# Kernel optimization log

Hardware: AMD Instinct MI355X
Metric: run time of the kernel (lower is better)

Reference implementation:

```python
import jax, jax.numpy as jnp
import numpy as np

ALPHA = 0.2  # LeakyReLU negative slope


def setup_inputs() -> dict:
    key = jax.random.key(0)
    k1, k2, k3, k4 = jax.random.split(key, 4)
    B, N, F_IN, F_OUT = 4, 4096, 256, 256
    h = jax.random.normal(k1, (B, N, F_IN), dtype=jnp.float32)
    adj = jax.random.randint(k2, (B, N, N), 0, 2, dtype=jnp.int32)
    # xavier_normal with gain=1.414: std = gain*sqrt(2/(fan_in+fan_out))
    std_W = 1.414 * np.sqrt(2.0 / (F_IN + F_OUT))
    W = jax.random.normal(k3, (F_IN, F_OUT), dtype=jnp.float32) * std_W
    std_a = 1.414 * np.sqrt(2.0 / (1 + 2 * F_OUT))
    a = jax.random.normal(k4, (1, 2 * F_OUT), dtype=jnp.float32) * std_a
    return {"h": h, "adj": adj, "W": W, "a": a}


def reference(h, adj, W, a):
    # h: [B, N, F_in], adj: [B, N, N] (0/1), W: [F_in, F_out], a: [1, 2*F_out]
    F_out = W.shape[1]
    Hh = jnp.einsum('bni,io->bno', h, W)               # [B, N, F_out]
    a_src = a[0, :F_out]                                # attends to edge source i
    a_dst = a[0, F_out:]                                # attends to edge target j
    s = jnp.einsum('bno,o->bn', Hh, a_src)              # [B, N]
    d = jnp.einsum('bno,o->bn', Hh, a_dst)              # [B, N]
    # score(i,j) = a . concat(Hh_i, Hh_j) = s_i + d_j
    logits = s[:, :, None] + d[:, None, :]              # [B, N, N]
    # edge_e = exp(-leakyrelu(score)) only on edges (adj nonzero), else 0
    e = jnp.where(adj != 0,
                  jnp.exp(-jax.nn.leaky_relu(logits, negative_slope=ALPHA)),
                  jnp.zeros((), dtype=Hh.dtype))        # [B, N, N]
    rowsum = jnp.sum(e, axis=-1, keepdims=True)         # [B, N, 1]
    # rows with zero sum keep divisor 1 (as in the torch code)
    rowsum = jnp.where(rowsum == 0.0, 1.0, rowsum)
    h_prime = jnp.einsum('bnm,bmo->bno', e, Hh) / rowsum  # [B, N, F_out]
    return jax.nn.elu(h_prime)  # concat=True branch
```

## Files before the change

kernel.cpp:

```cpp
#include <hip/hip_runtime.h>

#define LRELU_ALPHA 0.2f

typedef __bf16 bf16x8 __attribute__((ext_vector_type(8)));
typedef unsigned short u16;
typedef unsigned short u16x4v __attribute__((ext_vector_type(4)));
typedef unsigned short u16x8 __attribute__((ext_vector_type(8)));
typedef float f32x4 __attribute__((ext_vector_type(4)));
typedef int int4v __attribute__((ext_vector_type(4)));
typedef unsigned int u32;
typedef unsigned long long u64;

__device__ __forceinline__ u16 f2bf(float f) {
  unsigned int u = __float_as_uint(f);
  u += 0x7fffu + ((u >> 16) & 1u);
  return (u16)(u >> 16);
}

__device__ __forceinline__ void gload16(const void* g, void* lds) {
  __builtin_amdgcn_global_load_lds(
      (const __attribute__((address_space(1))) void*)g,
      (__attribute__((address_space(3))) void*)lds, 16, 0, 0);
}

__global__ __launch_bounds__(256) void wcast(const float* __restrict__ W,
                                             u16* __restrict__ WbT) {
  int idx = blockIdx.x * 256 + threadIdx.x;
  WbT[idx] = f2bf(W[(idx & 255) * 256 + (idx >> 8)]);
}

__global__ __launch_bounds__(256) void packadj(const int* __restrict__ adj,
                                               u32* __restrict__ maskg) {
  const int tid = threadIdx.x;
  const int l = tid & 63, w = tid >> 6;
  const size_t row = (size_t)blockIdx.x * 4 + w;
  const int* arow = adj + row * 4096;
  u64* mrow = (u64*)(maskg + row * 128);
  for (int it = 0; it < 16; ++it) {
    const int* base = arow + it * 256;
    int v0 = base[l], v1 = base[l + 64], v2 = base[l + 128], v3 = base[l + 192];
    u64 b0 = __ballot(v0 != 0);
    u64 b1 = __ballot(v1 != 0);
    u64 b2 = __ballot(v2 != 0);
    u64 b3 = __ballot(v3 != 0);
    if (l == 0) {
      mrow[it * 4 + 0] = b0;
      mrow[it * 4 + 1] = b1;
      mrow[it * 4 + 2] = b2;
      mrow[it * 4 + 3] = b3;
    }
  }
}

__global__ __launch_bounds__(256) void gemm1(const float* __restrict__ h,
                                             const u16* __restrict__ WbT,
                                             const float* __restrict__ a,
                                             u16* __restrict__ HhTt,
                                             float* __restrict__ sbuf,
                                             float* __restrict__ dbuf) {
  const int tid = threadIdx.x, bid = blockIdx.x;
  const int l = tid & 63, w = tid >> 6;
  const int lr = l & 15;
  const int lk = (l >> 4) << 3;
  const int rowA = bid * 64 + 16 * w + lr;
  const float* hrow = h + (size_t)rowA * 256 + lk;

  f32x4 acc[16];
#pragma unroll
  for (int n = 0; n < 16; ++n) acc[n] = (f32x4){0.f, 0.f, 0.f, 0.f};

  for (int k0 = 0; k0 < 256; k0 += 32) {
    f32x4 a0 = *(const f32x4*)(hrow + k0);
    f32x4 a1 = *(const f32x4*)(hrow + k0 + 4);
    u16x8 au;
    au[0] = f2bf(a0[0]); au[1] = f2bf(a0[1]); au[2] = f2bf(a0[2]); au[3] = f2bf(a0[3]);
    au[4] = f2bf(a1[0]); au[5] = f2bf(a1[1]); au[6] = f2bf(a1[2]); au[7] = f2bf(a1[3]);
    bf16x8 af = __builtin_bit_cast(bf16x8, au);
#pragma unroll
    for (int n = 0; n < 16; ++n) {
      int4v bv = *(const int4v*)(WbT + (size_t)(16 * n + lr) * 256 + k0 + lk);
      bf16x8 bf = __builtin_bit_cast(bf16x8, bv);
      acc[n] = __builtin_amdgcn_mfma_f32_16x16x32_bf16(af, bf, acc[n], 0, 0, 0);
    }
  }

  float sp[4] = {0.f, 0.f, 0.f, 0.f}, dp[4] = {0.f, 0.f, 0.f, 0.f};
#pragma unroll
  for (int n = 0; n < 16; ++n) {
    int col = 16 * n + lr;
    float as = a[col];
    float ad = a[256 + col];
#pragma unroll
    for (int rr = 0; rr < 4; ++rr) {
      int row = bid * 64 + 16 * w + ((l >> 4) << 2) + rr;
      int bb = row >> 12, kk = row & 4095;
      float v = acc[n][rr];
      size_t addr = (size_t)bb * 1048576 + (size_t)(kk >> 5) * 8192 +
                    (col >> 4) * 512 + ((kk >> 3) & 3) * 128 + (col & 15) * 8 +
                    (kk & 7);
      HhTt[addr] = f2bf(v);
      sp[rr] += v * as;
      dp[rr] += v * ad;
    }
  }
#pragma unroll
  for (int rr = 0; rr < 4; ++rr) {
#pragma unroll
    for (int off = 1; off < 16; off <<= 1) {
      sp[rr] += __shfl_xor(sp[rr], off);
      dp[rr] += __shfl_xor(dp[rr], off);
    }
  }
  if ((l & 15) == 0) {
#pragma unroll
    for (int rr = 0; rr < 4; ++rr) {
      int row = bid * 64 + 16 * w + ((l >> 4) << 2) + rr;
      sbuf[row] = sp[rr];
      dbuf[row] = dp[rr];
    }
  }
}

__global__ __launch_bounds__(256, 2) void gat_main(const u32* __restrict__ maskg,
                                                   const u16* __restrict__ HhTt,
                                                   const float* __restrict__ s,
                                                   const float* __restrict__ d,
                                                   float* __restrict__ out) {
  __shared__ __align__(16) u16 Bt[3][8192];
  __shared__ __align__(16) u16 At[2][1024];
  __shared__ __align__(16) u32 Mk[4096];
  __shared__ __align__(16) float Dt[3][32];
  __shared__ float rs_lds[32];

  const int tid = threadIdx.x, bid = blockIdx.x;
  const int xcd = bid & 7;
  const int t512 = (xcd << 6) | (bid >> 3);
  const int b = t512 >> 7;
  const int rowbase = (t512 & 127) << 5;

  const int l = tid & 63, w = tid >> 6;
  const int lr = l & 15, lkg = l >> 4;
  const int er = tid >> 3, c8 = tid & 7;

  {
    const u32* mrow = maskg + ((size_t)(b * 4096 + rowbase)) * 128;
    const int r = tid >> 3;
    const int w0 = (tid & 7) * 16;
#pragma unroll
    for (int j = 0; j < 16; ++j) {
      int ww = w0 + j;
      Mk[r * 128 + ((ww + r) & 127)] = mrow[r * 128 + ww];
    }
  }

  const float s_e = s[b * 4096 + rowbase + er];

  const char* bsrcB = (const char*)HhTt + (size_t)b * 2097152 + l * 16;
  const char* dsrcB = (const char*)d + (size_t)b * 16384 + w * 32 + l * 16;
  char* BtB = (char*)&Bt[0][0];
  char* DtB = (char*)&Dt[0][0];

  const int atoff0 = lr * 32 + lkg * 8;
  const int atoff1 = (16 + lr) * 32 + lkg * 8;
  const int btbase = (w * 4) * 512 + lkg * 128 + lr * 8;

  f32x4 acc0[4], acc1[4];
#pragma unroll
  for (int n = 0; n < 4; ++n) {
    acc0[n] = (f32x4){0.f, 0.f, 0.f, 0.f};
    acc1[n] = (f32x4){0.f, 0.f, 0.f, 0.f};
  }
  float racc = 0.f;

#define ISSUE_B(BUF, STEP)                                                    \
  {                                                                           \
    const size_t so_ = (size_t)(STEP) * 16384;                                \
    gload16(bsrcB + so_ + (w * 4 + 0) * 1024,                                 \
            BtB + (BUF) * 16384 + (w * 4 + 0) * 1024);                        \
    gload16(bsrcB + so_ + (w * 4 + 1) * 1024,                                 \
            BtB + (BUF) * 16384 + (w * 4 + 1) * 1024);                        \
    gload16(bsrcB + so_ + (w * 4 + 2) * 1024,                                 \
            BtB + (BUF) * 16384 + (w * 4 + 2) * 1024);                        \
    gload16(bsrcB + so_ + (w * 4 + 3) * 1024,                                 \
            BtB + (BUF) * 16384 + (w * 4 + 3) * 1024);                        \
  }

#define ISSUE_D(STEP)                                                         \
  {                                                                           \
    const int dst_ = (STEP) > 127 ? 127 : (STEP);                             \
    if (l < 2) gload16(dsrcB + (size_t)dst_ * 128,                            \
                       DtB + (dst_ % 3) * 128 + w * 32 + l * 16);             \
  }

#define EGEN(BA, STEP)                                                        \
  {                                                                           \
    u32 mword = Mk[er * 128 + (((STEP) + er) & 127)];                         \
    u32 m4 = mword >> (c8 * 4);                                               \
    f32x4 dv = *(const f32x4*)(DtB + ((STEP) % 3) * 128 + c8 * 16);           \
    u16x4v ev;                                                                \
    _Pragma("unroll")                                                         \
    for (int j = 0; j < 4; ++j) {                                             \
      float lg = s_e + dv[j];                                                 \
      float t = fmaxf(lg, LRELU_ALPHA * lg);                                  \
      float e = ((m4 >> j) & 1) ? __expf(-t) : 0.f;                           \
      racc += e;                                                              \
      ev[j] = f2bf(e);                                                        \
    }                                                                         \
    *(u16x4v*)&At[BA][er * 32 + c8 * 4] = ev;                                 \
  }

#define COMPUTE(BB, BA)                                                       \
  {                                                                           \
    bf16x8 af0 = __builtin_bit_cast(bf16x8, *(const int4v*)&At[BA][atoff0]);  \
    bf16x8 af1 = __builtin_bit_cast(bf16x8, *(const int4v*)&At[BA][atoff1]);  \
    __builtin_amdgcn_s_setprio(1);                                            \
    _Pragma("unroll")                                                         \
    for (int n = 0; n < 4; ++n) {                                             \
      bf16x8 bfv = __builtin_bit_cast(bf16x8,                                 \
          *(const int4v*)&Bt[BB][btbase + n * 512]);                          \
      acc0[n] = __builtin_amdgcn_mfma_f32_16x16x32_bf16(af0, bfv, acc0[n],    \
                                                        0, 0, 0);             \
      acc1[n] = __builtin_amdgcn_mfma_f32_16x16x32_bf16(af1, bfv, acc1[n],    \
                                                        0, 0, 0);             \
    }                                                                         \
    __builtin_amdgcn_s_setprio(0);                                            \
  }

#define SUBSTEP(J, BB, BA, BI, BAN)                                           \
  {                                                                           \
    ISSUE_B(BI, (J) + 2)                                                      \
    ISSUE_D((J) + 3)                                                          \
    EGEN(BAN, (J) + 1)                                                        \
    COMPUTE(BB, BA)                                                           \
    asm volatile("s_waitcnt lgkmcnt(0)" ::: "memory");                        \
    asm volatile("s_waitcnt vmcnt(5)" ::: "memory");                          \
    __builtin_amdgcn_s_barrier();                                             \
  }

  ISSUE_B(0, 0)
  ISSUE_B(1, 1)
  ISSUE_D(1)
  ISSUE_D(2)
  f32x4 d0v = *(const f32x4*)(d + b * 4096 + c8 * 4);
  __syncthreads();
  {
    u32 mword = Mk[er * 128 + (er & 127)];
    u32 m4 = mword >> (c8 * 4);
    u16x4v ev;
#pragma unroll
    for (int j = 0; j < 4; ++j) {
      float lg = s_e + d0v[j];
      float t = fmaxf(lg, LRELU_ALPHA * lg);
      float e = ((m4 >> j) & 1) ? __expf(-t) : 0.f;
      racc += e;
      ev[j] = f2bf(e);
    }
    *(u16x4v*)&At[0][er * 32 + c8 * 4] = ev;
  }
  asm volatile("s_waitcnt lgkmcnt(0)" ::: "memory");
  __builtin_amdgcn_s_barrier();

  for (int k = 0; k < 126; k += 6) {
    SUBSTEP(k + 0, 0, 0, 2, 1)
    SUBSTEP(k + 1, 1, 1, 0, 0)
    SUBSTEP(k + 2, 2, 0, 1, 1)
    SUBSTEP(k + 3, 0, 1, 2, 0)
    SUBSTEP(k + 4, 1, 0, 0, 1)
    SUBSTEP(k + 5, 2, 1, 1, 0)
  }
  EGEN(1, 127)
  COMPUTE(0, 0)
  asm volatile("s_waitcnt lgkmcnt(0)" ::: "memory");
  asm volatile("s_waitcnt vmcnt(0)" ::: "memory");
  __builtin_amdgcn_s_barrier();
  COMPUTE(1, 1)
#undef ISSUE_B
#undef ISSUE_D
#undef EGEN
#undef COMPUTE
#undef SUBSTEP

  racc += __shfl_xor(racc, 1);
  racc += __shfl_xor(racc, 2);
  racc += __shfl_xor(racc, 4);
  if (c8 == 0) rs_lds[er] = (racc == 0.f) ? 1.f : racc;
  __syncthreads();

#pragma unroll
  for (int t16 = 0; t16 < 2; ++t16) {
#pragma unroll
    for (int n = 0; n < 4; ++n) {
#pragma unroll
      for (int reg = 0; reg < 4; ++reg) {
        int rloc = 16 * t16 + lkg * 4 + reg;
        int col = w * 64 + 16 * n + lr;
        float v = (t16 ? acc1[n][reg] : acc0[n][reg]) / rs_lds[rloc];
        out[((size_t)(b * 4096 + rowbase + rloc)) * 256 + col] =
            v > 0.f ? v : (__expf(v) - 1.f);
      }
    }
  }
}

extern "C" void kernel_launch(void* const* d_in, const int* in_sizes, int n_in,
                              void* d_out, int out_size, void* d_ws, size_t ws_size,
                              hipStream_t stream) {
  const float* h = (const float*)d_in[0];
  const int* adj = (const int*)d_in[1];
  const float* W = (const float*)d_in[2];
  const float* a = (const float*)d_in[3];
  float* out = (float*)d_out;

  u16* WbT   = (u16*)d_ws;
  u16* HhTt  = (u16*)((char*)d_ws + 131072);
  float* sb  = (float*)((char*)d_ws + 131072 + 8388608);
  float* db  = sb + 16384;
  u32* maskg = (u32*)((char*)d_ws + 131072 + 8388608 + 131072);

  hipLaunchKernelGGL(wcast,    dim3(256),  dim3(256), 0, stream, W, WbT);
  hipLaunchKernelGGL(packadj,  dim3(4096), dim3(256), 0, stream, adj, maskg);
  hipLaunchKernelGGL(gemm1,    dim3(256),  dim3(256), 0, stream, h, WbT, a, HhTt, sb, db);
  hipLaunchKernelGGL(gat_main, dim3(512),  dim3(256), 0, stream, maskg, HhTt, sb, db, out);
}
```

Baseline: 170.2 us.

## Retile attention kernel to 64-row by 128-column panels and merge W cast into adjacency packing

The main attention kernel now tiles each block as 64 rows by 128 output columns instead of 32 rows by 256 columns. Each block computes twice as many attention weights per column-half, and each thread builds 8 weights per step. The change halves the B-tile staging per step and enlarges the mask and A buffers, trading duplicated exp work across the two column halves for less feature-tile traffic and a different LDS footprint. The W transpose/cast kernel is also folded into the adjacency-packing launch as extra blocks, removing one kernel launch.

```diff
diff --git a/kernel.cpp b/kernel.cpp
--- a/kernel.cpp
+++ b/kernel.cpp
@@ -4,7 +4,6 @@
 
 typedef __bf16 bf16x8 __attribute__((ext_vector_type(8)));
 typedef unsigned short u16;
-typedef unsigned short u16x4v __attribute__((ext_vector_type(4)));
 typedef unsigned short u16x8 __attribute__((ext_vector_type(8)));
 typedef float f32x4 __attribute__((ext_vector_type(4)));
 typedef int int4v __attribute__((ext_vector_type(4)));
@@ -23,15 +22,16 @@
       (__attribute__((address_space(3))) void*)lds, 16, 0, 0);
 }
 
-__global__ __launch_bounds__(256) void wcast(const float* __restrict__ W,
+__global__ __launch_bounds__(256) void packw(const int* __restrict__ adj,
+                                             u32* __restrict__ maskg,
+                                             const float* __restrict__ W,
                                              u16* __restrict__ WbT) {
-  int idx = blockIdx.x * 256 + threadIdx.x;
-  WbT[idx] = f2bf(W[(idx & 255) * 256 + (idx >> 8)]);
-}
-
-__global__ __launch_bounds__(256) void packadj(const int* __restrict__ adj,
-                                               u32* __restrict__ maskg) {
   const int tid = threadIdx.x;
+  if (blockIdx.x >= 4096) {
+    int idx = (blockIdx.x - 4096) * 256 + tid;
+    WbT[idx] = f2bf(W[(idx & 255) * 256 + (idx >> 8)]);
+    return;
+  }
   const int l = tid & 63, w = tid >> 6;
   const size_t row = (size_t)blockIdx.x * 4 + w;
   const int* arow = adj + row * 4096;
@@ -126,28 +126,30 @@
                                                    const float* __restrict__ s,
                                                    const float* __restrict__ d,
                                                    float* __restrict__ out) {
-  __shared__ __align__(16) u16 Bt[3][8192];
-  __shared__ __align__(16) u16 At[2][1024];
-  __shared__ __align__(16) u32 Mk[4096];
+  __shared__ __align__(16) u16 Bt[3][4096];
+  __shared__ __align__(16) u16 At[2][2048];
+  __shared__ __align__(16) u32 Mk[8192];
   __shared__ __align__(16) float Dt[3][32];
-  __shared__ float rs_lds[32];
+  __shared__ float rs_lds[64];
 
   const int tid = threadIdx.x, bid = blockIdx.x;
   const int xcd = bid & 7;
-  const int t512 = (xcd << 6) | (bid >> 3);
-  const int b = t512 >> 7;
-  const int rowbase = (t512 & 127) << 5;
+  const int t = ((xcd & 1) << 6) | (bid >> 3);
+  const int b = xcd >> 1;
+  const int rowpanel = t >> 1, ch = t & 1;
+  const int rowbase = rowpanel << 6;
 
   const int l = tid & 63, w = tid >> 6;
   const int lr = l & 15, lkg = l >> 4;
-  const int er = tid >> 3, c8 = tid & 7;
+  const int wr = w & 1, wc = w >> 1;
+  const int er = tid >> 2, c4 = tid & 3;
 
   {
     const u32* mrow = maskg + ((size_t)(b * 4096 + rowbase)) * 128;
-    const int r = tid >> 3;
-    const int w0 = (tid & 7) * 16;
-#pragma unroll
-    for (int j = 0; j < 16; ++j) {
+    const int r = tid >> 2;
+    const int w0 = (tid & 3) * 32;
+#pragma unroll
+    for (int j = 0; j < 32; ++j) {
       int ww = w0 + j;
       Mk[r * 128 + ((ww + r) & 127)] = mrow[r * 128 + ww];
     }
@@ -155,14 +157,14 @@
 
   const float s_e = s[b * 4096 + rowbase + er];
 
-  const char* bsrcB = (const char*)HhTt + (size_t)b * 2097152 + l * 16;
+  const char* bsrcB = (const char*)HhTt + (size_t)b * 2097152 + ch * 8192 + l * 16;
   const char* dsrcB = (const char*)d + (size_t)b * 16384 + w * 32 + l * 16;
   char* BtB = (char*)&Bt[0][0];
   char* DtB = (char*)&Dt[0][0];
 
-  const int atoff0 = lr * 32 + lkg * 8;
-  const int atoff1 = (16 + lr) * 32 + lkg * 8;
-  const int btbase = (w * 4) * 512 + lkg * 128 + lr * 8;
+  const int atoff0 = (32 * wr + lr) * 32 + lkg * 8;
+  const int atoff1 = (32 * wr + 16 + lr) * 32 + lkg * 8;
+  const int btbase = 4 * wc * 512 + lkg * 128 + lr * 8;
 
   f32x4 acc0[4], acc1[4];
 #pragma unroll
@@ -175,14 +177,10 @@
 #define ISSUE_B(BUF, STEP)                                                    \
   {                                                                           \
     const size_t so_ = (size_t)(STEP) * 16384;                                \
-    gload16(bsrcB + so_ + (w * 4 + 0) * 1024,                                 \
-            BtB + (BUF) * 16384 + (w * 4 + 0) * 1024);                        \
-    gload16(bsrcB + so_ + (w * 4 + 1) * 1024,                                 \
-            BtB + (BUF) * 16384 + (w * 4 + 1) * 1024);                        \
-    gload16(bsrcB + so_ + (w * 4 + 2) * 1024,                                 \
-            BtB + (BUF) * 16384 + (w * 4 + 2) * 1024);                        \
-    gload16(bsrcB + so_ + (w * 4 + 3) * 1024,                                 \
-            BtB + (BUF) * 16384 + (w * 4 + 3) * 1024);                        \
+    gload16(bsrcB + so_ + (w * 2 + 0) * 1024,                                 \
+            BtB + (BUF) * 8192 + (w * 2 + 0) * 1024);                         \
+    gload16(bsrcB + so_ + (w * 2 + 1) * 1024,                                 \
+            BtB + (BUF) * 8192 + (w * 2 + 1) * 1024);                         \
   }
 
 #define ISSUE_D(STEP)                                                         \
@@ -195,18 +193,19 @@
 #define EGEN(BA, STEP)                                                        \
   {                                                                           \
     u32 mword = Mk[er * 128 + (((STEP) + er) & 127)];                         \
-    u32 m4 = mword >> (c8 * 4);                                               \
-    f32x4 dv = *(const f32x4*)(DtB + ((STEP) % 3) * 128 + c8 * 16);           \
-    u16x4v ev;                                                                \
+    u32 m8 = mword >> (c4 * 8);                                               \
+    f32x4 dvA = *(const f32x4*)(DtB + ((STEP) % 3) * 128 + c4 * 32);          \
+    f32x4 dvB = *(const f32x4*)(DtB + ((STEP) % 3) * 128 + c4 * 32 + 16);     \
+    u16x8 ev;                                                                 \
     _Pragma("unroll")                                                         \
-    for (int j = 0; j < 4; ++j) {                                             \
-      float lg = s_e + dv[j];                                                 \
-      float t = fmaxf(lg, LRELU_ALPHA * lg);                                  \
-      float e = ((m4 >> j) & 1) ? __expf(-t) : 0.f;                           \
+    for (int j = 0; j < 8; ++j) {                                             \
+      float lg = s_e + (j < 4 ? dvA[j & 3] : dvB[j & 3]);                     \
+      float tt = fmaxf(lg, LRELU_ALPHA * lg);                                 \
+      float e = ((m8 >> j) & 1) ? __expf(-tt) : 0.f;                          \
       racc += e;                                                              \
       ev[j] = f2bf(e);                                                        \
     }                                                                         \
-    *(u16x4v*)&At[BA][er * 32 + c8 * 4] = ev;                                 \
+    *(int4v*)&At[BA][er * 32 + c4 * 8] = __builtin_bit_cast(int4v, ev);       \
   }
 
 #define COMPUTE(BB, BA)                                                       \
@@ -233,7 +232,7 @@
     EGEN(BAN, (J) + 1)                                                        \
     COMPUTE(BB, BA)                                                           \
     asm volatile("s_waitcnt lgkmcnt(0)" ::: "memory");                        \
-    asm volatile("s_waitcnt vmcnt(5)" ::: "memory");                          \
+    asm volatile("s_waitcnt vmcnt(3)" ::: "memory");                          \
     __builtin_amdgcn_s_barrier();                                             \
   }
 
@@ -241,21 +240,22 @@
   ISSUE_B(1, 1)
   ISSUE_D(1)
   ISSUE_D(2)
-  f32x4 d0v = *(const f32x4*)(d + b * 4096 + c8 * 4);
+  f32x4 d0A = *(const f32x4*)(d + b * 4096 + c4 * 8);
+  f32x4 d0B = *(const f32x4*)(d + b * 4096 + c4 * 8 + 4);
   __syncthreads();
   {
     u32 mword = Mk[er * 128 + (er & 127)];
-    u32 m4 = mword >> (c8 * 4);
-    u16x4v ev;
-#pragma unroll
-    for (int j = 0; j < 4; ++j) {
-      float lg = s_e + d0v[j];
-      float t = fmaxf(lg, LRELU_ALPHA * lg);
-      float e = ((m4 >> j) & 1) ? __expf(-t) : 0.f;
+    u32 m8 = mword >> (c4 * 8);
+    u16x8 ev;
+#pragma unroll
+    for (int j = 0; j < 8; ++j) {
+      float lg = s_e + (j < 4 ? d0A[j & 3] : d0B[j & 3]);
+      float tt = fmaxf(lg, LRELU_ALPHA * lg);
+      float e = ((m8 >> j) & 1) ? __expf(-tt) : 0.f;
       racc += e;
       ev[j] = f2bf(e);
     }
-    *(u16x4v*)&At[0][er * 32 + c8 * 4] = ev;
+    *(int4v*)&At[0][er * 32 + c4 * 8] = __builtin_bit_cast(int4v, ev);
   }
   asm volatile("s_waitcnt lgkmcnt(0)" ::: "memory");
   __builtin_amdgcn_s_barrier();
@@ -282,8 +282,7 @@
 
   racc += __shfl_xor(racc, 1);
   racc += __shfl_xor(racc, 2);
-  racc += __shfl_xor(racc, 4);
-  if (c8 == 0) rs_lds[er] = (racc == 0.f) ? 1.f : racc;
+  if (c4 == 0) rs_lds[er] = (racc == 0.f) ? 1.f : racc;
   __syncthreads();
 
 #pragma unroll
@@ -292,8 +291,8 @@
     for (int n = 0; n < 4; ++n) {
 #pragma unroll
       for (int reg = 0; reg < 4; ++reg) {
-        int rloc = 16 * t16 + lkg * 4 + reg;
-        int col = w * 64 + 16 * n + lr;
+        int rloc = 32 * wr + 16 * t16 + lkg * 4 + reg;
+        int col = ch * 128 + wc * 64 + 16 * n + lr;
         float v = (t16 ? acc1[n][reg] : acc0[n][reg]) / rs_lds[rloc];
         out[((size_t)(b * 4096 + rowbase + rloc)) * 256 + col] =
             v > 0.f ? v : (__expf(v) - 1.f);
@@ -317,8 +316,7 @@
   float* db  = sb + 16384;
   u32* maskg = (u32*)((char*)d_ws + 131072 + 8388608 + 131072);
 
-  hipLaunchKernelGGL(wcast,    dim3(256),  dim3(256), 0, stream, W, WbT);
-  hipLaunchKernelGGL(packadj,  dim3(4096), dim3(256), 0, stream, adj, maskg);
+  hipLaunchKernelGGL(packw,    dim3(4352), dim3(256), 0, stream, adj, maskg, W, WbT);
   hipLaunchKernelGGL(gemm1,    dim3(256),  dim3(256), 0, stream, h, WbT, a, HhTt, sb, db);
   hipLaunchKernelGGL(gat_main, dim3(512),  dim3(256), 0, stream, maskg, HhTt, sb, db, out);
 }
```

New measurement: 173.9 us. 2.2% more time.
